# Kernel optimization log

Measured on AMD Instinct MI355X. Metric: run time of the kernel, lower is better.

## Reference

```python
import jax, jax.numpy as jnp
import numpy as np
import math

N_NODES = 50000
N_EDGES = 800000
D = 128
ALPHA = 0.1
BETA = 0.5


def setup_inputs() -> dict:
    key = jax.random.key(0)
    k = jax.random.split(key, 7)
    h = jax.random.normal(k[0], (N_NODES, D), dtype=jnp.float32)
    h0 = jax.random.normal(k[1], (N_NODES, D), dtype=jnp.float32)
    edge_row = jnp.sort(jax.random.randint(k[2], (N_EDGES,), 0, N_NODES, dtype=jnp.int32))
    edge_col = jax.random.randint(k[3], (N_EDGES,), 0, N_NODES, dtype=jnp.int32)
    edge_vals = jax.random.uniform(k[4], (N_EDGES,), dtype=jnp.float32)
    # nn.Linear(input_dim, output_dim): W is [out, in], b is [out]
    bound = 1.0 / math.sqrt(D)
    W = jax.random.uniform(k[5], (D, D), minval=-bound, maxval=bound, dtype=jnp.float32)
    b = jax.random.uniform(k[6], (D,), minval=-bound, maxval=bound, dtype=jnp.float32)
    return {"h": h, "h0": h0, "edge_row": edge_row, "edge_col": edge_col,
            "edge_vals": edge_vals, "W": W, "b": b, "l": 4}


def reference(h, h0, edge_row, edge_col, edge_vals, W, b, l):
    theta = math.log(BETA / l + 1.0)
    # sparse adj @ h : gather source features, scale by edge value, scatter-add to rows
    msgs = edge_vals[:, None] * h[edge_col]          # [E, D]
    hi = jax.ops.segment_sum(msgs, edge_row, num_segments=N_NODES)  # [N, D]
    support = (1.0 - ALPHA) * hi + ALPHA * h0
    lin = support @ W.T + b
    return theta * lin + (1.0 - theta) * support
```

## Files before the change

### kernel.cpp

```cpp
#include <hip/hip_runtime.h>
#include <hip/hip_bf16.h>
#include <math.h>

#define NN 50000
#define DD 128
#define ALPHA 0.1f
#define BETA 0.5f

typedef __attribute__((ext_vector_type(8))) short short8;
typedef __attribute__((ext_vector_type(4))) float floatx4;
typedef _Float16 h2 __attribute__((ext_vector_type(2)));

__device__ __forceinline__ float bf16lo(unsigned u) {
    return __uint_as_float(u << 16);
}
__device__ __forceinline__ float bf16hi(unsigned u) {
    return __uint_as_float(u & 0xffff0000u);
}
__device__ __forceinline__ unsigned pkh(float a, float b) {
    h2 p = {(_Float16)a, (_Float16)b};
    return __builtin_bit_cast(unsigned, p);
}
__device__ __forceinline__ h2 as_h2(unsigned u) {
    return __builtin_bit_cast(h2, u);
}

__global__ __launch_bounds__(256) void prep_kernel(
    const int* __restrict__ edge_row, int E, int* __restrict__ rp,
    const float* __restrict__ h, ushort* __restrict__ hh,
    const float* __restrict__ W, ushort* __restrict__ wf)
{
    const int t = blockIdx.x * 256 + threadIdx.x;

    if (hh != nullptr && t < NN * DD / 8) {
        const float4 v0 = *reinterpret_cast<const float4*>(h + (size_t)t * 8);
        const float4 v1 = *reinterpret_cast<const float4*>(h + (size_t)t * 8 + 4);
        uint4 o;
        o.x = pkh(v0.x, v0.y);
        o.y = pkh(v0.z, v0.w);
        o.z = pkh(v1.x, v1.y);
        o.w = pkh(v1.z, v1.w);
        *reinterpret_cast<uint4*>(hh + (size_t)t * 8) = o;
    }

    if (wf != nullptr && t < DD * DD / 4) {
        const float4 v = *reinterpret_cast<const float4*>(W + (size_t)t * 4);
        uint2 of;
        of.x = pkh(v.x, v.y);
        of.y = pkh(v.z, v.w);
        *reinterpret_cast<uint2*>(wf + (size_t)t * 4) = of;
    }

    if (t <= E) {
        if (t == 0) {
            int r0 = edge_row[0];
            for (int r = 0; r <= r0; ++r) rp[r] = 0;
        } else if (t == E) {
            int rl = edge_row[E - 1];
            for (int r = rl + 1; r <= NN; ++r) rp[r] = E;
        } else {
            int rprev = edge_row[t - 1];
            int rcur  = edge_row[t];
            for (int r = rprev + 1; r <= rcur; ++r) rp[r] = t;
        }
    }
}

__global__ __launch_bounds__(512, 8) void fused8w(
    const ushort* __restrict__ hh, const float* __restrict__ h0,
    const int* __restrict__ edge_col, const float* __restrict__ edge_vals,
    const int* __restrict__ rp, const ushort* __restrict__ wf,
    const float* __restrict__ b, const int* __restrict__ lptr,
    float* __restrict__ out)
{
    __shared__ ushort sA[16][136];

    const int tid  = threadIdx.x;
    const int wave = tid >> 6;
    const int lane = tid & 63;
    const int g    = lane >> 4;
    const int li   = lane & 15;
    const int r0   = blockIdx.x * 16;
    const int rA   = r0 + wave * 2;
    const int rB   = rA + 1;

    const int lv = *lptr;
    const float theta  = logf(BETA / (float)lv + 1.0f);
    const float mtheta = 1.0f - theta;

    const int e0A = rp[rA], e1A = rp[rA + 1];
    const int e0B = rp[rB], e1B = rp[rB + 1];

    h2 aA0 = {0, 0}, aA1 = {0, 0}, aA2 = {0, 0}, aA3 = {0, 0};
    h2 aB0 = {0, 0}, aB1 = {0, 0}, aB2 = {0, 0}, aB3 = {0, 0};

    int ebA = e0A, ebB = e0B;
    const int mA = e0A + ((e1A - e0A) & ~15);
    const int mB = e0B + ((e1B - e0B) & ~15);

    for (; ebA < mA && ebB < mB; ebA += 16, ebB += 16) {
        #pragma unroll
        for (int u = 0; u < 4; ++u) {
            const int eA = ebA + u * 4 + g;
            const int cA = edge_col[eA];
            const float vA = edge_vals[eA];
            const uint4 hvA = *reinterpret_cast<const uint4*>(
                hh + (size_t)cA * DD + li * 8);

            const int eB = ebB + u * 4 + g;
            const int cB = edge_col[eB];
            const float vB = edge_vals[eB];
            const uint4 hvB = *reinterpret_cast<const uint4*>(
                hh + (size_t)cB * DD + li * 8);

            const _Float16 vhA = (_Float16)vA;
            const h2 vvA = {vhA, vhA};
            aA0 += as_h2(hvA.x) * vvA;
            aA1 += as_h2(hvA.y) * vvA;
            aA2 += as_h2(hvA.z) * vvA;
            aA3 += as_h2(hvA.w) * vvA;

            const _Float16 vhB = (_Float16)vB;
            const h2 vvB = {vhB, vhB};
            aB0 += as_h2(hvB.x) * vvB;
            aB1 += as_h2(hvB.y) * vvB;
            aB2 += as_h2(hvB.z) * vvB;
            aB3 += as_h2(hvB.w) * vvB;
        }
    }

    for (; ebA < mA; ebA += 16) {
        #pragma unroll
        for (int u = 0; u < 4; ++u) {
            const int eA = ebA + u * 4 + g;
            const int cA = edge_col[eA];
            const float vA = edge_vals[eA];
            const uint4 hvA = *reinterpret_cast<const uint4*>(
                hh + (size_t)cA * DD + li * 8);
            const _Float16 vhA = (_Float16)vA;
            const h2 vvA = {vhA, vhA};
            aA0 += as_h2(hvA.x) * vvA;
            aA1 += as_h2(hvA.y) * vvA;
            aA2 += as_h2(hvA.z) * vvA;
            aA3 += as_h2(hvA.w) * vvA;
        }
    }
    for (; ebB < mB; ebB += 16) {
        #pragma unroll
        for (int u = 0; u < 4; ++u) {
            const int eB = ebB + u * 4 + g;
            const int cB = edge_col[eB];
            const float vB = edge_vals[eB];
            const uint4 hvB = *reinterpret_cast<const uint4*>(
                hh + (size_t)cB * DD + li * 8);
            const _Float16 vhB = (_Float16)vB;
            const h2 vvB = {vhB, vhB};
            aB0 += as_h2(hvB.x) * vvB;
            aB1 += as_h2(hvB.y) * vvB;
            aB2 += as_h2(hvB.z) * vvB;
            aB3 += as_h2(hvB.w) * vvB;
        }
    }

    for (; ebA < e1A; ebA += 4) {
        const int e  = ebA + g;
        const int ee = min(e, e1A - 1);
        const int cA = edge_col[ee];
        const float vA = (e < e1A) ? edge_vals[ee] : 0.0f;
        const uint4 hvA = *reinterpret_cast<const uint4*>(
            hh + (size_t)cA * DD + li * 8);
        const _Float16 vhA = (_Float16)vA;
        const h2 vvA = {vhA, vhA};
        aA0 += as_h2(hvA.x) * vvA;
        aA1 += as_h2(hvA.y) * vvA;
        aA2 += as_h2(hvA.z) * vvA;
        aA3 += as_h2(hvA.w) * vvA;
    }
    for (; ebB < e1B; ebB += 4) {
        const int e  = ebB + g;
        const int ee = min(e, e1B - 1);
        const int cB = edge_col[ee];
        const float vB = (e < e1B) ? edge_vals[ee] : 0.0f;
        const uint4 hvB = *reinterpret_cast<const uint4*>(
            hh + (size_t)cB * DD + li * 8);
        const _Float16 vhB = (_Float16)vB;
        const h2 vvB = {vhB, vhB};
        aB0 += as_h2(hvB.x) * vvB;
        aB1 += as_h2(hvB.y) * vvB;
        aB2 += as_h2(hvB.z) * vvB;
        aB3 += as_h2(hvB.w) * vvB;
    }

    float accA[8], accB[8];
    accA[0] = (float)aA0.x; accA[1] = (float)aA0.y;
    accA[2] = (float)aA1.x; accA[3] = (float)aA1.y;
    accA[4] = (float)aA2.x; accA[5] = (float)aA2.y;
    accA[6] = (float)aA3.x; accA[7] = (float)aA3.y;
    accB[0] = (float)aB0.x; accB[1] = (float)aB0.y;
    accB[2] = (float)aB1.x; accB[3] = (float)aB1.y;
    accB[4] = (float)aB2.x; accB[5] = (float)aB2.y;
    accB[6] = (float)aB3.x; accB[7] = (float)aB3.y;

    #pragma unroll
    for (int j = 0; j < 8; ++j) {
        accA[j] += __shfl_xor(accA[j], 16);
        accA[j] += __shfl_xor(accA[j], 32);
        accB[j] += __shfl_xor(accB[j], 16);
        accB[j] += __shfl_xor(accB[j], 32);
    }

    if (g == 0) {
        {
            const float4 h0a = *reinterpret_cast<const float4*>(
                h0 + (size_t)rA * DD + li * 8);
            const float4 h0b = *reinterpret_cast<const float4*>(
                h0 + (size_t)rA * DD + li * 8 + 4);
            float s0 = fmaf(1.0f - ALPHA, accA[0], ALPHA * h0a.x);
            float s1 = fmaf(1.0f - ALPHA, accA[1], ALPHA * h0a.y);
            float s2 = fmaf(1.0f - ALPHA, accA[2], ALPHA * h0a.z);
            float s3 = fmaf(1.0f - ALPHA, accA[3], ALPHA * h0a.w);
            float s4 = fmaf(1.0f - ALPHA, accA[4], ALPHA * h0b.x);
            float s5 = fmaf(1.0f - ALPHA, accA[5], ALPHA * h0b.y);
            float s6 = fmaf(1.0f - ALPHA, accA[6], ALPHA * h0b.z);
            float s7 = fmaf(1.0f - ALPHA, accA[7], ALPHA * h0b.w);
            uint4 pk;
            pk.x = pkh(s0, s1);
            pk.y = pkh(s2, s3);
            pk.z = pkh(s4, s5);
            pk.w = pkh(s6, s7);
            *reinterpret_cast<uint4*>(&sA[wave * 2][li * 8]) = pk;
        }
        {
            const float4 h0a = *reinterpret_cast<const float4*>(
                h0 + (size_t)rB * DD + li * 8);
            const float4 h0b = *reinterpret_cast<const float4*>(
                h0 + (size_t)rB * DD + li * 8 + 4);
            float s0 = fmaf(1.0f - ALPHA, accB[0], ALPHA * h0a.x);
            float s1 = fmaf(1.0f - ALPHA, accB[1], ALPHA * h0a.y);
            float s2 = fmaf(1.0f - ALPHA, accB[2], ALPHA * h0a.z);
            float s3 = fmaf(1.0f - ALPHA, accB[3], ALPHA * h0a.w);
            float s4 = fmaf(1.0f - ALPHA, accB[4], ALPHA * h0b.x);
            float s5 = fmaf(1.0f - ALPHA, accB[5], ALPHA * h0b.y);
            float s6 = fmaf(1.0f - ALPHA, accB[6], ALPHA * h0b.z);
            float s7 = fmaf(1.0f - ALPHA, accB[7], ALPHA * h0b.w);
            uint4 pk;
            pk.x = pkh(s0, s1);
            pk.y = pkh(s2, s3);
            pk.z = pkh(s4, s5);
            pk.w = pkh(s6, s7);
            *reinterpret_cast<uint4*>(&sA[wave * 2 + 1][li * 8]) = pk;
        }
    }
    __syncthreads();

    const int la = lane & 15;
    const int k0 = (lane >> 4) * 8;
    const int c  = wave * 16 + la;

    floatx4 facc = (floatx4){0.f, 0.f, 0.f, 0.f};

    #pragma unroll
    for (int s = 0; s < 4; ++s) {
        const int k = s * 32 + k0;
        const short8 af = *reinterpret_cast<const short8*>(&sA[la][k]);
        const short8 bf = *reinterpret_cast<const short8*>(
            wf + (size_t)c * DD + k);
        facc = __builtin_amdgcn_mfma_f32_16x16x32_f16(af, bf, facc, 0, 0, 0);
    }

    const int rg = (lane >> 4) * 4;
    const float bb = b[c];
    #pragma unroll
    for (int j = 0; j < 4; ++j) {
        const int rl = rg + j;
        const float sup = (float)(*reinterpret_cast<const _Float16*>(&sA[rl][c]));
        out[(size_t)(r0 + rl) * DD + c] =
            theta * (facc[j] + bb) + mtheta * sup;
    }
}

__global__ __launch_bounds__(256, 6) void agg_fp32(
    const float* __restrict__ h, const float* __restrict__ h0,
    const int* __restrict__ edge_col, const float* __restrict__ edge_vals,
    const int* __restrict__ rp, float* __restrict__ io)
{
    const int wave = threadIdx.x >> 6;
    const int lane = threadIdx.x & 63;
    const int p    = lane >> 5;
    const int li   = lane & 31;
    const int r    = blockIdx.x * 4 + wave;
    if (r >= NN) return;

    const int e0 = rp[r], e1 = rp[r + 1];

    float4 A[4];
    #pragma unroll
    for (int u = 0; u < 4; ++u) A[u] = make_float4(0.f, 0.f, 0.f, 0.f);

    for (int eb = e0; eb < e1; eb += 8) {
        #pragma unroll
        for (int u = 0; u < 4; ++u) {
            const int e  = eb + 2 * u + p;
            const int ee = min(e, e1 - 1);
            const int   c = edge_col[ee];
            const float v = (e < e1) ? edge_vals[ee] : 0.0f;
            const float4 hv =
                *reinterpret_cast<const float4*>(h + (size_t)c * DD + li * 4);
            A[u].x = fmaf(v, hv.x, A[u].x);
            A[u].y = fmaf(v, hv.y, A[u].y);
            A[u].z = fmaf(v, hv.z, A[u].z);
            A[u].w = fmaf(v, hv.w, A[u].w);
        }
    }
    float4 s;
    s.x = (A[0].x + A[1].x) + (A[2].x + A[3].x);
    s.y = (A[0].y + A[1].y) + (A[2].y + A[3].y);
    s.z = (A[0].z + A[1].z) + (A[2].z + A[3].z);
    s.w = (A[0].w + A[1].w) + (A[2].w + A[3].w);
    s.x += __shfl_xor(s.x, 32);
    s.y += __shfl_xor(s.y, 32);
    s.z += __shfl_xor(s.z, 32);
    s.w += __shfl_xor(s.w, 32);

    if (p == 0) {
        const float4 h0v =
            *reinterpret_cast<const float4*>(h0 + (size_t)r * DD + li * 4);
        float4 sup;
        sup.x = fmaf(1.0f - ALPHA, s.x, ALPHA * h0v.x);
        sup.y = fmaf(1.0f - ALPHA, s.y, ALPHA * h0v.y);
        sup.z = fmaf(1.0f - ALPHA, s.z, ALPHA * h0v.z);
        sup.w = fmaf(1.0f - ALPHA, s.w, ALPHA * h0v.w);
        *reinterpret_cast<float4*>(io + (size_t)r * DD + li * 4) = sup;
    }
}

#define RPB 64
#define SPAD 132
#define WPAD 136

__global__ __launch_bounds__(512, 4) void lin_kernel(
    float* io, const float* __restrict__ W, const float* __restrict__ b,
    const int* __restrict__ lptr)
{
    __shared__ float sS[RPB][SPAD];
    __shared__ __hip_bfloat16 sWt[DD][WPAD];

    const int tid = threadIdx.x;
    const int r0  = blockIdx.x * RPB;
    const int tr  = tid >> 4;
    const int tc  = tid & 15;

    const int lv = *lptr;
    const float theta  = logf(BETA / (float)lv + 1.0f);
    const float mtheta = 1.0f - theta;

    for (int i = tid * 4; i < DD * DD; i += 512 * 4) {
        const float4 w4 = *reinterpret_cast<const float4*>(W + i);
        const int o = i >> 7;
        const int k = i & 127;
        sWt[k + 0][o] = __float2bfloat16(w4.x);
        sWt[k + 1][o] = __float2bfloat16(w4.y);
        sWt[k + 2][o] = __float2bfloat16(w4.z);
        sWt[k + 3][o] = __float2bfloat16(w4.w);
    }

    for (int idx = tid; idx < RPB * 32; idx += 512) {
        const int row = idx >> 5;
        const int q   = idx & 31;
        const int rr  = r0 + row;
        const float4 v = (rr < NN)
            ? *reinterpret_cast<const float4*>(io + (size_t)rr * DD + q * 4)
            : make_float4(0.f, 0.f, 0.f, 0.f);
        *reinterpret_cast<float4*>(&sS[row][q * 4]) = v;
    }
    __syncthreads();

    float acc[2][8];
    #pragma unroll
    for (int i = 0; i < 2; ++i)
        #pragma unroll
        for (int j = 0; j < 8; ++j) acc[i][j] = 0.f;

    for (int k = 0; k < DD; k += 4) {
        const float4 a0 = *reinterpret_cast<const float4*>(&sS[tr * 2 + 0][k]);
        const float4 a1 = *reinterpret_cast<const float4*>(&sS[tr * 2 + 1][k]);
        const float aa0[4] = {a0.x, a0.y, a0.z, a0.w};
        const float aa1[4] = {a1.x, a1.y, a1.z, a1.w};
        #pragma unroll
        for (int kk = 0; kk < 4; ++kk) {
            const uint4 wr = *reinterpret_cast<const uint4*>(&sWt[k + kk][tc * 8]);
            float w[8];
            w[0] = bf16lo(wr.x); w[1] = bf16hi(wr.x);
            w[2] = bf16lo(wr.y); w[3] = bf16hi(wr.y);
            w[4] = bf16lo(wr.z); w[5] = bf16hi(wr.z);
            w[6] = bf16lo(wr.w); w[7] = bf16hi(wr.w);
            #pragma unroll
            for (int j = 0; j < 8; ++j) {
                acc[0][j] = fmaf(aa0[kk], w[j], acc[0][j]);
                acc[1][j] = fmaf(aa1[kk], w[j], acc[1][j]);
            }
        }
    }

    #pragma unroll
    for (int i = 0; i < 2; ++i) {
        const int ri = tr * 2 + i;
        const int rr = r0 + ri;
        if (rr >= NN) continue;
        #pragma unroll
        for (int j4 = 0; j4 < 2; ++j4) {
            const int cc = tc * 8 + j4 * 4;
            const float4 bv  = *reinterpret_cast<const float4*>(&b[cc]);
            const float4 sup = *reinterpret_cast<const float4*>(&sS[ri][cc]);
            float4 o4;
            o4.x = theta * (acc[i][j4 * 4 + 0] + bv.x) + mtheta * sup.x;
            o4.y = theta * (acc[i][j4 * 4 + 1] + bv.y) + mtheta * sup.y;
            o4.z = theta * (acc[i][j4 * 4 + 2] + bv.z) + mtheta * sup.z;
            o4.w = theta * (acc[i][j4 * 4 + 3] + bv.w) + mtheta * sup.w;
            *reinterpret_cast<float4*>(io + (size_t)rr * DD + cc) = o4;
        }
    }
}

extern "C" void kernel_launch(void* const* d_in, const int* in_sizes, int n_in,
                              void* d_out, int out_size, void* d_ws, size_t ws_size,
                              hipStream_t stream) {
    const float* h         = (const float*)d_in[0];
    const float* h0        = (const float*)d_in[1];
    const int*   edge_row  = (const int*)d_in[2];
    const int*   edge_col  = (const int*)d_in[3];
    const float* edge_vals = (const float*)d_in[4];
    const float* W         = (const float*)d_in[5];
    const float* b         = (const float*)d_in[6];
    const int*   lptr      = (const int*)d_in[7];
    const int E = in_sizes[2];

    char* wsb = (char*)d_ws;
    const size_t sz_hh = (size_t)NN * DD * sizeof(ushort);
    const size_t sz_w  = (size_t)DD * DD * sizeof(ushort);
    int*    rp = (int*)wsb;
    ushort* hh = (ushort*)(wsb + (1 << 18));
    ushort* wf = (ushort*)(wsb + (1 << 18) + sz_hh);
    float*  io = (float*)d_out;

    const size_t need = (size_t)(1 << 18) + sz_hh + sz_w;

    const int nT = (NN * DD / 8 > E + 1) ? NN * DD / 8 : E + 1;
    const int gridP = (nT + 255) / 256;

    if (ws_size >= need) {
        prep_kernel<<<gridP, 256, 0, stream>>>(edge_row, E, rp, h, hh, W, wf);
        fused8w<<<NN / 16, 512, 0, stream>>>(
            hh, h0, edge_col, edge_vals, rp, wf, b, lptr, io);
    } else {
        prep_kernel<<<gridP, 256, 0, stream>>>(edge_row, E, rp, h,
                                               nullptr, W, nullptr);
        agg_fp32<<<(NN + 3) / 4, 256, 0, stream>>>(h, h0, edge_col, edge_vals, rp, io);
        lin_kernel<<<(NN + RPB - 1) / RPB, 512, 0, stream>>>(io, W, b, lptr);
    }
}
```

Baseline: 63.08 us.

## Make linear stage per-wave to drop block barrier, keep fp32 support

Each wave now runs the 128-wide linear layer on its own two rows with MFMA, masking 14 of the 16 A rows to zero. This lets a wave barrier replace the block-wide __syncthreads, and blocks shrink to 256 threads covering 8 rows. The support term is also kept in fp32 shared memory for the residual instead of being re-read as fp16. The cost is eight times more MFMA work and eight times more W loads per row, since most of each MFMA tile is padding.

```diff
diff --git a/kernel.cpp b/kernel.cpp
--- a/kernel.cpp
+++ b/kernel.cpp
@@ -66,22 +66,22 @@
     }
 }
 
-__global__ __launch_bounds__(512, 8) void fused8w(
+__global__ __launch_bounds__(256, 8) void fused2r(
     const ushort* __restrict__ hh, const float* __restrict__ h0,
     const int* __restrict__ edge_col, const float* __restrict__ edge_vals,
     const int* __restrict__ rp, const ushort* __restrict__ wf,
     const float* __restrict__ b, const int* __restrict__ lptr,
     float* __restrict__ out)
 {
-    __shared__ ushort sA[16][136];
+    __shared__ ushort sAf[4][2][136];
+    __shared__ float  sSf[4][2][132];
 
     const int tid  = threadIdx.x;
     const int wave = tid >> 6;
     const int lane = tid & 63;
     const int g    = lane >> 4;
     const int li   = lane & 15;
-    const int r0   = blockIdx.x * 16;
-    const int rA   = r0 + wave * 2;
+    const int rA   = blockIdx.x * 8 + wave * 2;
     const int rB   = rA + 1;
 
     const int lv = *lptr;
@@ -223,12 +223,16 @@
             float s5 = fmaf(1.0f - ALPHA, accA[5], ALPHA * h0b.y);
             float s6 = fmaf(1.0f - ALPHA, accA[6], ALPHA * h0b.z);
             float s7 = fmaf(1.0f - ALPHA, accA[7], ALPHA * h0b.w);
+            *reinterpret_cast<float4*>(&sSf[wave][0][li * 8]) =
+                make_float4(s0, s1, s2, s3);
+            *reinterpret_cast<float4*>(&sSf[wave][0][li * 8 + 4]) =
+                make_float4(s4, s5, s6, s7);
             uint4 pk;
             pk.x = pkh(s0, s1);
             pk.y = pkh(s2, s3);
             pk.z = pkh(s4, s5);
             pk.w = pkh(s6, s7);
-            *reinterpret_cast<uint4*>(&sA[wave * 2][li * 8]) = pk;
+            *reinterpret_cast<uint4*>(&sAf[wave][0][li * 8]) = pk;
         }
         {
             const float4 h0a = *reinterpret_cast<const float4*>(
@@ -243,39 +247,51 @@
             float s5 = fmaf(1.0f - ALPHA, accB[5], ALPHA * h0b.y);
             float s6 = fmaf(1.0f - ALPHA, accB[6], ALPHA * h0b.z);
             float s7 = fmaf(1.0f - ALPHA, accB[7], ALPHA * h0b.w);
+            *reinterpret_cast<float4*>(&sSf[wave][1][li * 8]) =
+                make_float4(s0, s1, s2, s3);
+            *reinterpret_cast<float4*>(&sSf[wave][1][li * 8 + 4]) =
+                make_float4(s4, s5, s6, s7);
             uint4 pk;
             pk.x = pkh(s0, s1);
             pk.y = pkh(s2, s3);
             pk.z = pkh(s4, s5);
             pk.w = pkh(s6, s7);
-            *reinterpret_cast<uint4*>(&sA[wave * 2 + 1][li * 8]) = pk;
-        }
-    }
-    __syncthreads();
+            *reinterpret_cast<uint4*>(&sAf[wave][1][li * 8]) = pk;
+        }
+    }
+    __builtin_amdgcn_wave_barrier();
 
     const int la = lane & 15;
     const int k0 = (lane >> 4) * 8;
-    const int c  = wave * 16 + la;
-
-    floatx4 facc = (floatx4){0.f, 0.f, 0.f, 0.f};
-
+    const int rowsel = min(la, 1);
+    const bool valid = (la < 2);
+
+    short8 af[4];
     #pragma unroll
     for (int s = 0; s < 4; ++s) {
-        const int k = s * 32 + k0;
-        const short8 af = *reinterpret_cast<const short8*>(&sA[la][k]);
-        const short8 bf = *reinterpret_cast<const short8*>(
-            wf + (size_t)c * DD + k);
-        facc = __builtin_amdgcn_mfma_f32_16x16x32_f16(af, bf, facc, 0, 0, 0);
+        const short8 v = *reinterpret_cast<const short8*>(
+            &sAf[wave][rowsel][s * 32 + k0]);
+        af[s] = valid ? v : (short8){0, 0, 0, 0, 0, 0, 0, 0};
     }
 
     const int rg = (lane >> 4) * 4;
-    const float bb = b[c];
-    #pragma unroll
-    for (int j = 0; j < 4; ++j) {
-        const int rl = rg + j;
-        const float sup = (float)(*reinterpret_cast<const _Float16*>(&sA[rl][c]));
-        out[(size_t)(r0 + rl) * DD + c] =
-            theta * (facc[j] + bb) + mtheta * sup;
+    #pragma unroll
+    for (int t = 0; t < 8; ++t) {
+        const int c = t * 16 + la;
+        floatx4 facc = (floatx4){0.f, 0.f, 0.f, 0.f};
+        #pragma unroll
+        for (int s = 0; s < 4; ++s) {
+            const short8 bf = *reinterpret_cast<const short8*>(
+                wf + (size_t)c * DD + s * 32 + k0);
+            facc = __builtin_amdgcn_mfma_f32_16x16x32_f16(af[s], bf, facc, 0, 0, 0);
+        }
+        if (rg == 0) {
+            const float bb = b[c];
+            out[(size_t)rA * DD + c] =
+                theta * (facc[0] + bb) + mtheta * sSf[wave][0][c];
+            out[(size_t)rB * DD + c] =
+                theta * (facc[1] + bb) + mtheta * sSf[wave][1][c];
+        }
     }
 }
 
@@ -450,7 +466,7 @@
 
     if (ws_size >= need) {
         prep_kernel<<<gridP, 256, 0, stream>>>(edge_row, E, rp, h, hh, W, wf);
-        fused8w<<<NN / 16, 512, 0, stream>>>(
+        fused2r<<<(NN + 7) / 8, 256, 0, stream>>>(
             hh, h0, edge_col, edge_vals, rp, wf, b, lptr, io);
     } else {
         prep_kernel<<<gridP, 256, 0, stream>>>(edge_row, E, rp, h,
```

After: 132.0 us. 2.09x slower.
